# Optimization experiments

Hardware: AMD Instinct MI355X
Metric: run time of the kernel (lower is better)

Reference implementation:

```python
import jax, jax.numpy as jnp
import numpy as np

DIM = 1024
CTX_DIM = 768
H = 16


def setup_inputs() -> dict:
    key = jax.random.key(0)
    k1, k2, k3, k4, k5 = jax.random.split(key, 5)
    x = jax.random.normal(k1, (2, 2048, DIM), dtype=jnp.float32)
    context = jax.random.normal(k2, (2, 2048, CTX_DIM), dtype=jnp.float32)
    # Linear weights stored as [in, out] (y = x @ W); no biases per module.
    s = 0.02
    Wq = jax.random.normal(k3, (DIM, DIM), dtype=jnp.float32) * s
    Wkv = jax.random.normal(k4, (CTX_DIM, 2 * DIM), dtype=jnp.float32) * s
    Wo = jax.random.normal(k5, (DIM, DIM), dtype=jnp.float32) * s
    return {"x": x, "context": context, "Wq": Wq, "Wkv": Wkv, "Wo": Wo}


def reference(x, context, Wq, Wkv, Wo):
    B, N, C = x.shape
    Dh = C // H  # head dim
    scale = Dh ** -0.5
    M = context.shape[1]
    q = (x @ Wq).reshape(B, N, H, Dh).transpose(0, 2, 1, 3)      # [B,H,N,Dh]
    kv = context @ Wkv                                            # [B,M,2C]
    k, v = jnp.split(kv, 2, axis=-1)
    k = k.reshape(B, M, H, Dh).transpose(0, 2, 1, 3)              # [B,H,M,Dh]
    v = v.reshape(B, M, H, Dh).transpose(0, 2, 1, 3)              # [B,H,M,Dh]
    attn = jax.nn.softmax(jnp.einsum('bhnd,bhmd->bhnm', q, k) * scale, axis=-1)
    out = jnp.einsum('bhnm,bhmd->bhnd', attn, v)                  # [B,H,N,Dh]
    out = out.transpose(0, 2, 1, 3).reshape(B, N, C)
    return out @ Wo  # dropout is identity in eval / p=0
```

## Files before the change

### kernel.cpp

```cpp
#include <hip/hip_runtime.h>

typedef __attribute__((ext_vector_type(4))) float f32x4;
typedef __attribute__((ext_vector_type(8))) short short8;
typedef __attribute__((ext_vector_type(4))) unsigned int u32x4;
typedef unsigned short u16;
typedef unsigned int u32;
typedef unsigned long long u64;

__device__ __forceinline__ u16 f2bf(float f) {
  u32 u = __builtin_bit_cast(u32, f);
  u += 0x7fffu + ((u >> 16) & 1u);
  return (u16)(u >> 16);
}
__device__ __forceinline__ u16 f2bf_t(float f) {
  return (u16)(__builtin_bit_cast(u32, f) >> 16);
}

__device__ __forceinline__ void gl2lds16(const u16* g, const u16* l) {
  __builtin_amdgcn_global_load_lds(
      (const __attribute__((address_space(1))) u32*)g,
      (__attribute__((address_space(3))) u32*)(u32)(u64)l,
      16, 0, 0);
}

__device__ __forceinline__ void cast_body(const float* __restrict__ s,
                                          u16* __restrict__ d, int blk,
                                          int tid) {
  long i = (long)blk * 256 + tid;
  const f32x4* sp = (const f32x4*)(s + i * 8);
  f32x4 a = sp[0], b = sp[1];
  u16 t[8];
#pragma unroll
  for (int j = 0; j < 4; j++) {
    t[j] = f2bf(a[j]);
    t[4 + j] = f2bf(b[j]);
  }
  *(u32x4*)(d + i * 8) = *(u32x4*)t;
}

__device__ __forceinline__ void transpose_body(const float* __restrict__ W,
                                               u16* __restrict__ WT, int K,
                                               int N, int k0, int n0, int tid,
                                               u16* T) {
#pragma unroll
  for (int i = 0; i < 4; i++) {
    int c = tid + 256 * i;
    int row = c >> 4;
    int ch = c & 15;
    f32x4 f = *(const f32x4*)(W + (long)(k0 + row) * N + n0 + ch * 4);
#pragma unroll
    for (int j = 0; j < 4; j++) T[(ch * 4 + j) * 72 + row] = f2bf(f[j]);
  }
  __syncthreads();
#pragma unroll
  for (int i = 0; i < 2; i++) {
    int c = tid + 256 * i;
    int row = c >> 3;
    int ch = c & 7;
    u32x4 v = *(u32x4*)&T[row * 72 + ch * 8];
    *(u32x4*)(WT + (long)(n0 + row) * K + k0 + ch * 8) = v;
  }
}

__global__ __launch_bounds__(256) void prep(
    const float* __restrict__ x, const float* __restrict__ ctx,
    const float* __restrict__ Wq, const float* __restrict__ Wkv,
    const float* __restrict__ Wo, u16* __restrict__ xb,
    u16* __restrict__ ctxb, u16* __restrict__ wqT, u16* __restrict__ wkvT,
    u16* __restrict__ woT) {
  __shared__ __align__(16) u16 T[64 * 72];
  const int b = blockIdx.x, tid = threadIdx.x;
  if (b < 2048) {
    cast_body(x, xb, b, tid);
  } else if (b < 3584) {
    cast_body(ctx, ctxb, b - 2048, tid);
  } else if (b < 3840) {
    int idx = b - 3584;
    transpose_body(Wq, wqT, 1024, 1024, (idx >> 4) * 64, (idx & 15) * 64, tid, T);
  } else if (b < 4224) {
    int idx = b - 3840;
    transpose_body(Wkv, wkvT, 768, 2048, (idx >> 5) * 64, (idx & 31) * 64, tid, T);
  } else {
    int idx = b - 4224;
    transpose_body(Wo, woT, 1024, 1024, (idx >> 4) * 64, (idx & 15) * 64, tid, T);
  }
}

__device__ __forceinline__ void gemm128_core(
    const u16* __restrict__ A, const u16* __restrict__ Bt, int Kstride,
    int Klen, long brow, long bcol, int tid, u16* As, u16* Bs,
    f32x4 (&acc)[4][4]) {
  const int lane = tid & 63, wv = tid >> 6;
  const int l15 = lane & 15, quad = lane >> 4;
  const int wr = (wv >> 1) * 64, wc = (wv & 1) * 64;
  const int sr = lane >> 3, sc = lane & 7;
  const int csw = ((sc ^ sr) & 7) * 8;

  const u16* ag[4];
  const u16* bg[4];
  const u16* al[4];
  const u16* bl[4];
#pragma unroll
  for (int n = 0; n < 4; n++) {
    int row = wv * 32 + n * 8;
    ag[n] = A + (brow + row + sr) * (long)Kstride + csw;
    al[n] = &As[row * 64];
    bg[n] = Bt + (bcol + row + sr) * (long)Kstride + csw;
    bl[n] = &Bs[row * 64];
  }

  for (int kt = 0; kt < Klen; kt += 64) {
    __syncthreads();
#pragma unroll
    for (int n = 0; n < 4; n++) gl2lds16(ag[n] + kt, al[n]);
#pragma unroll
    for (int n = 0; n < 4; n++) gl2lds16(bg[n] + kt, bl[n]);
    __syncthreads();
#pragma unroll
    for (int kk = 0; kk < 2; kk++) {
      short8 af[4], bf[4];
#pragma unroll
      for (int i = 0; i < 4; i++) {
        int row = wr + i * 16 + l15;
        af[i] = *(short8*)&As[row * 64 + (((kk * 4 + quad) ^ (row & 7)) << 3)];
      }
#pragma unroll
      for (int j = 0; j < 4; j++) {
        int row = wc + j * 16 + l15;
        bf[j] = *(short8*)&Bs[row * 64 + (((kk * 4 + quad) ^ (row & 7)) << 3)];
      }
#pragma unroll
      for (int i = 0; i < 4; i++)
#pragma unroll
        for (int j = 0; j < 4; j++)
          acc[i][j] = __builtin_amdgcn_mfma_f32_16x16x32_bf16(
              af[i], bf[j], acc[i][j], 0, 0, 0);
    }
  }
}

__global__ __launch_bounds__(256, 3) void fused_qkv(
    const u16* __restrict__ xb, const u16* __restrict__ ctxb,
    const u16* __restrict__ wqT, const u16* __restrict__ wkvT,
    u16* __restrict__ Qb, u16* __restrict__ Kfrag, u16* __restrict__ Vfrag,
    float qscale) {
  __shared__ __align__(16) u16 As[128 * 64];
  __shared__ __align__(16) u16 Bs[128 * 64];
  const int tid = threadIdx.x;
  const int lane = tid & 63, wv = tid >> 6;
  const int l15 = lane & 15, quad = lane >> 4;
  const int wr = (wv >> 1) * 64, wc = (wv & 1) * 64;

  f32x4 acc[4][4];
#pragma unroll
  for (int i = 0; i < 4; i++)
#pragma unroll
    for (int j = 0; j < 4; j++) acc[i][j] = (f32x4){0.f, 0.f, 0.f, 0.f};

  int bid = blockIdx.x;
  if (bid < 256) {
    long brow = (long)(bid >> 3) * 128, bcol = (long)(bid & 7) * 128;
    gemm128_core(xb, wqT, 1024, 1024, brow, bcol, tid, As, Bs, acc);
#pragma unroll
    for (int i = 0; i < 4; i++)
#pragma unroll
      for (int j = 0; j < 4; j++)
#pragma unroll
        for (int r = 0; r < 4; r++) {
          long row = brow + wr + i * 16 + quad * 4 + r;
          long col = bcol + wc + j * 16 + l15;
          Qb[row * 1024 + col] = f2bf(acc[i][j][r] * qscale);
        }
    return;
  }

  bid -= 256;
  long brow = (long)(bid >> 4) * 128, bcol = (long)(bid & 15) * 128;
  gemm128_core(ctxb, wkvT, 768, 768, brow, bcol, tid, As, Bs, acc);

  const bool is_k = (bcol < 1024);
  __syncthreads();
#pragma unroll
  for (int round = 0; round < 2; round++) {
    if ((wv >> 1) == round) {
      if (is_k) {
#pragma unroll
        for (int i = 0; i < 4; i++)
#pragma unroll
          for (int j = 0; j < 4; j++) {
            int d = j * 16 + l15;
            int off = (wv & 1) * 4096 + ((d >> 5) * 4 + i) * 512 +
                      (((d >> 3) & 3) * 16 + quad * 4) * 8 + (d & 7);
#pragma unroll
            for (int r = 0; r < 4; r++) As[off + r * 8] = f2bf(acc[i][j][r]);
          }
      } else {
#pragma unroll
        for (int i = 0; i < 4; i++)
#pragma unroll
          for (int j = 0; j < 4; j++) {
            int off = (wv & 1) * 4096 + ((i >> 1) * 4 + j) * 512 +
                      (quad * 16 + l15) * 8 + (i & 1) * 4;
            u16 t4[4];
#pragma unroll
            for (int r = 0; r < 4; r++) t4[r] = f2bf(acc[i][j][r]);
            *(u64*)&As[off] = *(const u64*)t4;
          }
      }
    }
    __syncthreads();
    long mg = brow + round * 64;
    int b_ = (int)(mg >> 11), mt = (int)((mg >> 6) & 31);
#pragma unroll
    for (int h2 = 0; h2 < 2; h2++) {
      int h = (int)((is_k ? bcol : bcol - 1024) >> 6) + h2;
      u16* dst = (is_k ? Kfrag : Vfrag) + ((long)(b_ * 16 + h) * 32 + mt) * 4096;
#pragma unroll
      for (int p = 0; p < 2; p++) {
        int c = p * 256 + tid;
        *(u32x4*)(dst + c * 8) = *(u32x4*)&As[h2 * 4096 + c * 8];
      }
    }
    __syncthreads();
  }
}

__global__ __launch_bounds__(256, 3) void gemm_o(
    const u16* __restrict__ A, const u16* __restrict__ Bt,
    float* __restrict__ C) {
  __shared__ __align__(16) u16 As[128 * 64];
  __shared__ __align__(16) u16 Bs[128 * 64];
  const int tid = threadIdx.x;
  const int lane = tid & 63, wv = tid >> 6;
  const int l15 = lane & 15, quad = lane >> 4;
  const int wr = (wv >> 1) * 64, wc = (wv & 1) * 64;
  long brow = (long)blockIdx.y * 128, bcol = (long)blockIdx.x * 128;

  f32x4 acc[4][4];
#pragma unroll
  for (int i = 0; i < 4; i++)
#pragma unroll
    for (int j = 0; j < 4; j++) acc[i][j] = (f32x4){0.f, 0.f, 0.f, 0.f};

  gemm128_core(A, Bt, 1024, 1024, brow, bcol, tid, As, Bs, acc);

#pragma unroll
  for (int i = 0; i < 4; i++)
#pragma unroll
    for (int j = 0; j < 4; j++)
#pragma unroll
      for (int r = 0; r < 4; r++) {
        long row = brow + wr + i * 16 + quad * 4 + r;
        long col = bcol + wc + j * 16 + l15;
        C[row * 1024 + col] = acc[i][j][r];
      }
}

__global__ __launch_bounds__(512, 4) void attn_kernel(
    const u16* __restrict__ Q, const u16* __restrict__ Kfrag,
    const u16* __restrict__ Vfrag, u16* __restrict__ AO) {
  __shared__ __align__(16) u16 smem[2][4][4096];
  const int tid = threadIdx.x;
  const int lane = tid & 63, wv = tid >> 6;
  const int qc = wv & 3, half = wv >> 2;
  const int l15 = lane & 15, quad = lane >> 4;
  const int bh = blockIdx.y;
  const int b = bh >> 4, h = bh & 15;
  const long qrow0 = (long)b * 2048 + blockIdx.x * 128 + qc * 32;

  short8 qf[2][2];
#pragma unroll
  for (int qt = 0; qt < 2; qt++)
#pragma unroll
    for (int kk = 0; kk < 2; kk++)
      qf[qt][kk] = *(const short8*)&Q[(qrow0 + qt * 16 + l15) * 1024 +
                                      h * 64 + kk * 32 + quad * 8];

  f32x4 O[2][5];
#pragma unroll
  for (int qt = 0; qt < 2; qt++)
#pragma unroll
    for (int dt = 0; dt < 5; dt++) O[qt][dt] = (f32x4){0.f, 0.f, 0.f, 0.f};

  u32x4 ones_u = {0x3F803F80u, 0x3F803F80u, 0x3F803F80u, 0x3F803F80u};
  short8 ones = __builtin_bit_cast(short8, ones_u);

  const u16* kg0 = Kfrag + (long)bh * 32 * 4096;
  const u16* vg0 = Vfrag + (long)bh * 32 * 4096;
  const int so = wv * 512 + lane * 8;

  auto stage = [&](int nb, int i) {
    const u16* k0 = kg0 + (long)i * 4096 + so;
    const u16* v0 = vg0 + (long)i * 4096 + so;
    gl2lds16(k0, &smem[nb][0][wv * 512]);
    gl2lds16(v0, &smem[nb][1][wv * 512]);
    gl2lds16(k0 + 16 * 4096, &smem[nb][2][wv * 512]);
    gl2lds16(v0 + 16 * 4096, &smem[nb][3][wv * 512]);
  };

  stage(0, 0);
  __syncthreads();

  for (int i = 0; i < 16; i++) {
    const int cur = i & 1;
    if (i < 15) stage(cur ^ 1, i + 1);

    const u16* Ks = &smem[cur][half * 2][0] + lane * 8;
    const u16* Vs = &smem[cur][half * 2 + 1][0] + lane * 8;

    f32x4 s[4][2];
#pragma unroll
    for (int m4 = 0; m4 < 4; m4++)
#pragma unroll
      for (int qt = 0; qt < 2; qt++) s[m4][qt] = (f32x4){0.f, 0.f, 0.f, 0.f};
#pragma unroll
    for (int kk = 0; kk < 2; kk++) {
      short8 kf[4];
#pragma unroll
      for (int t = 0; t < 4; t++)
        kf[t] = *(const short8*)(Ks + (kk * 4 + t) * 512);
#pragma unroll
      for (int m4 = 0; m4 < 4; m4++)
#pragma unroll
        for (int qt = 0; qt < 2; qt++)
          s[m4][qt] = __builtin_amdgcn_mfma_f32_16x16x32_bf16(
              kf[m4], qf[qt][kk], s[m4][qt], 0, 0, 0);
    }

#pragma unroll
    for (int kk = 0; kk < 2; kk++) {
      short8 vf[4];
#pragma unroll
      for (int dt = 0; dt < 4; dt++)
        vf[dt] = *(const short8*)(Vs + (kk * 4 + dt) * 512);
#pragma unroll
      for (int qt = 0; qt < 2; qt++) {
        u32 w[4];
#pragma unroll
        for (int hw = 0; hw < 2; hw++) {
          f32x4 sv = s[2 * kk + hw][qt];
          u32 lo = (u32)f2bf_t(__builtin_amdgcn_exp2f(sv[0] - 24.f)) |
                   ((u32)f2bf_t(__builtin_amdgcn_exp2f(sv[1] - 24.f)) << 16);
          u32 hi = (u32)f2bf_t(__builtin_amdgcn_exp2f(sv[2] - 24.f)) |
                   ((u32)f2bf_t(__builtin_amdgcn_exp2f(sv[3] - 24.f)) << 16);
          w[hw * 2] = lo;
          w[hw * 2 + 1] = hi;
        }
        short8 pa = __builtin_bit_cast(short8, *(u32x4*)w);
#pragma unroll
        for (int dt = 0; dt < 4; dt++)
          O[qt][dt] = __builtin_amdgcn_mfma_f32_16x16x32_bf16(
              pa, vf[dt], O[qt][dt], 0, 0, 0);
        O[qt][4] = __builtin_amdgcn_mfma_f32_16x16x32_bf16(
            pa, ones, O[qt][4], 0, 0, 0);
      }
    }
    __syncthreads();
  }

  f32x4* cb = (f32x4*)&smem[0][0][0];
  if (half) {
#pragma unroll
    for (int qt = 0; qt < 2; qt++)
#pragma unroll
      for (int dt = 0; dt < 5; dt++)
        cb[(qc * 64 + lane) * 10 + qt * 5 + dt] = O[qt][dt];
  }
  __syncthreads();
  if (!half) {
#pragma unroll
    for (int qt = 0; qt < 2; qt++)
#pragma unroll
      for (int dt = 0; dt < 5; dt++)
        O[qt][dt] += cb[(qc * 64 + lane) * 10 + qt * 5 + dt];

#pragma unroll
    for (int qt = 0; qt < 2; qt++) {
      float inv[4];
#pragma unroll
      for (int r = 0; r < 4; r++) inv[r] = 1.f / O[qt][4][r];
#pragma unroll
      for (int dt = 0; dt < 4; dt++)
#pragma unroll
        for (int r = 0; r < 4; r++) {
          long row = qrow0 + qt * 16 + quad * 4 + r;
          int col = h * 64 + dt * 16 + l15;
          AO[row * 1024 + col] = f2bf(O[qt][dt][r] * inv[r]);
        }
    }
  }
}

extern "C" void kernel_launch(void* const* d_in, const int* in_sizes, int n_in,
                              void* d_out, int out_size, void* d_ws,
                              size_t ws_size, hipStream_t stream) {
  const float* x = (const float*)d_in[0];
  const float* ctx = (const float*)d_in[1];
  const float* Wq = (const float*)d_in[2];
  const float* Wkv = (const float*)d_in[3];
  const float* Wo = (const float*)d_in[4];
  float* out = (float*)d_out;

  u16* ws = (u16*)d_ws;
  u16* wqT = ws;
  u16* wkvT = wqT + 1048576;
  u16* woT = wkvT + 1572864;
  u16* Qb = woT + 1048576;
  u16* Kfrag = Qb + 4194304;
  u16* Vfrag = Kfrag + 4194304;
  u16* xb = Vfrag + 4194304;
  u16* ctxb = xb + 4194304;
  u16* AOb = xb;

  const float qscale = 0.125f * 1.4426950408889634f;

  prep<<<dim3(4480), 256, 0, stream>>>(x, ctx, Wq, Wkv, Wo, xb, ctxb, wqT,
                                       wkvT, woT);

  fused_qkv<<<dim3(768), 256, 0, stream>>>(xb, ctxb, wqT, wkvT, Qb, Kfrag,
                                           Vfrag, qscale);

  attn_kernel<<<dim3(16, 32), 512, 0, stream>>>(Qb, Kfrag, Vfrag, AOb);

  gemm_o<<<dim3(8, 32), 256, 0, stream>>>(AOb, woT, out);
}
```

Measured before the change: 178.1 us.

## Deepen attention K/V staging to four-buffer ring with finer steps

Restructures the attention loop from 16 double-buffered iterations into 32 half-sized steps over a 4-slot LDS ring, with three stages kept in flight. Each step waits on a manual vmcnt counter and a raw barrier instead of a full __syncthreads. It also wraps the MFMA bursts in s_setprio and packs the bf16 truncation with v_perm. The aim is to hide global-to-LDS load latency and lower synchronization stalls, at the cost of fragile manual waitcnt bookkeeping. LDS usage stays the same.

```diff
diff --git a/kernel.cpp b/kernel.cpp
--- a/kernel.cpp
+++ b/kernel.cpp
@@ -259,7 +259,7 @@
 __global__ __launch_bounds__(512, 4) void attn_kernel(
     const u16* __restrict__ Q, const u16* __restrict__ Kfrag,
     const u16* __restrict__ Vfrag, u16* __restrict__ AO) {
-  __shared__ __align__(16) u16 smem[2][4][4096];
+  __shared__ __align__(16) u16 smem[4][8192];
   const int tid = threadIdx.x;
   const int lane = tid & 63, wv = tid >> 6;
   const int qc = wv & 3, half = wv >> 2;
@@ -287,78 +287,102 @@
 
   const u16* kg0 = Kfrag + (long)bh * 32 * 4096;
   const u16* vg0 = Vfrag + (long)bh * 32 * 4096;
-  const int so = wv * 512 + lane * 8;
-
-  auto stage = [&](int nb, int i) {
-    const u16* k0 = kg0 + (long)i * 4096 + so;
-    const u16* v0 = vg0 + (long)i * 4096 + so;
-    gl2lds16(k0, &smem[nb][0][wv * 512]);
-    gl2lds16(v0, &smem[nb][1][wv * 512]);
-    gl2lds16(k0 + 16 * 4096, &smem[nb][2][wv * 512]);
-    gl2lds16(v0 + 16 * 4096, &smem[nb][3][wv * 512]);
+
+  auto stage = [&](int s) {
+#pragma unroll
+    for (int u = 0; u < 2; u++) {
+      int c = wv * 2 + u;
+      int g3 = c >> 2, idx = c & 3;
+      int hh = g3 >> 1;
+      const u16* src;
+      if ((g3 & 1) == 0) {
+        int kk = idx >> 1, tt = idx & 1;
+        src = kg0 + (long)(hh * 16 + (s >> 1)) * 4096 +
+              (kk * 4 + (s & 1) * 2 + tt) * 512 + lane * 8;
+      } else {
+        src = vg0 + (long)(hh * 16 + (s >> 1)) * 4096 +
+              ((s & 1) * 4 + idx) * 512 + lane * 8;
+      }
+      gl2lds16(src, &smem[s & 3][c * 512]);
+    }
   };
 
-  stage(0, 0);
-  __syncthreads();
-
-  for (int i = 0; i < 16; i++) {
-    const int cur = i & 1;
-    if (i < 15) stage(cur ^ 1, i + 1);
-
-    const u16* Ks = &smem[cur][half * 2][0] + lane * 8;
-    const u16* Vs = &smem[cur][half * 2 + 1][0] + lane * 8;
-
-    f32x4 s[4][2];
-#pragma unroll
-    for (int m4 = 0; m4 < 4; m4++)
-#pragma unroll
-      for (int qt = 0; qt < 2; qt++) s[m4][qt] = (f32x4){0.f, 0.f, 0.f, 0.f};
-#pragma unroll
-    for (int kk = 0; kk < 2; kk++) {
-      short8 kf[4];
-#pragma unroll
-      for (int t = 0; t < 4; t++)
-        kf[t] = *(const short8*)(Ks + (kk * 4 + t) * 512);
-#pragma unroll
-      for (int m4 = 0; m4 < 4; m4++)
+  stage(0);
+  stage(1);
+  stage(2);
+
+  for (int s = 0; s < 32; s++) {
+    if (s < 30)
+      asm volatile("s_waitcnt vmcnt(4)" ::: "memory");
+    else if (s == 30)
+      asm volatile("s_waitcnt vmcnt(2)" ::: "memory");
+    else
+      asm volatile("s_waitcnt vmcnt(0)" ::: "memory");
+    __builtin_amdgcn_s_barrier();
+    asm volatile("" ::: "memory");
+    if (s + 3 < 32) stage(s + 3);
+
+    const u16* rb = &smem[s & 3][0];
+    const u16* Ks = rb + half * 4096 + lane * 8;
+    const u16* Vs = rb + half * 4096 + 2048 + lane * 8;
+
+    short8 kf[2][2];
+#pragma unroll
+    for (int kk = 0; kk < 2; kk++)
+#pragma unroll
+      for (int tt = 0; tt < 2; tt++)
+        kf[kk][tt] = *(const short8*)(Ks + (kk * 2 + tt) * 512);
+    f32x4 sacc[2][2];
+#pragma unroll
+    for (int tt = 0; tt < 2; tt++)
+#pragma unroll
+      for (int qt = 0; qt < 2; qt++) sacc[tt][qt] = (f32x4){0.f, 0.f, 0.f, 0.f};
+    __builtin_amdgcn_s_setprio(1);
+#pragma unroll
+    for (int kk = 0; kk < 2; kk++)
+#pragma unroll
+      for (int tt = 0; tt < 2; tt++)
 #pragma unroll
         for (int qt = 0; qt < 2; qt++)
-          s[m4][qt] = __builtin_amdgcn_mfma_f32_16x16x32_bf16(
-              kf[m4], qf[qt][kk], s[m4][qt], 0, 0, 0);
-    }
-
-#pragma unroll
-    for (int kk = 0; kk < 2; kk++) {
-      short8 vf[4];
+          sacc[tt][qt] = __builtin_amdgcn_mfma_f32_16x16x32_bf16(
+              kf[kk][tt], qf[qt][kk], sacc[tt][qt], 0, 0, 0);
+    __builtin_amdgcn_s_setprio(0);
+
+    short8 pa[2];
+#pragma unroll
+    for (int qt = 0; qt < 2; qt++) {
+      u32 w[4];
+#pragma unroll
+      for (int tt = 0; tt < 2; tt++) {
+        f32x4 sv = sacc[tt][qt];
+        u32 e0 = __builtin_bit_cast(u32, __builtin_amdgcn_exp2f(sv[0] - 24.f));
+        u32 e1 = __builtin_bit_cast(u32, __builtin_amdgcn_exp2f(sv[1] - 24.f));
+        u32 e2 = __builtin_bit_cast(u32, __builtin_amdgcn_exp2f(sv[2] - 24.f));
+        u32 e3 = __builtin_bit_cast(u32, __builtin_amdgcn_exp2f(sv[3] - 24.f));
+        w[tt * 2] = __builtin_amdgcn_perm(e1, e0, 0x07060302u);
+        w[tt * 2 + 1] = __builtin_amdgcn_perm(e3, e2, 0x07060302u);
+      }
+      pa[qt] = __builtin_bit_cast(short8, *(u32x4*)w);
+    }
+
+    short8 vf[4];
+#pragma unroll
+    for (int dt = 0; dt < 4; dt++)
+      vf[dt] = *(const short8*)(Vs + dt * 512);
+    __builtin_amdgcn_s_setprio(1);
+#pragma unroll
+    for (int qt = 0; qt < 2; qt++) {
 #pragma unroll
       for (int dt = 0; dt < 4; dt++)
-        vf[dt] = *(const short8*)(Vs + (kk * 4 + dt) * 512);
-#pragma unroll
-      for (int qt = 0; qt < 2; qt++) {
-        u32 w[4];
-#pragma unroll
-        for (int hw = 0; hw < 2; hw++) {
-          f32x4 sv = s[2 * kk + hw][qt];
-          u32 lo = (u32)f2bf_t(__builtin_amdgcn_exp2f(sv[0] - 24.f)) |
-                   ((u32)f2bf_t(__builtin_amdgcn_exp2f(sv[1] - 24.f)) << 16);
-          u32 hi = (u32)f2bf_t(__builtin_amdgcn_exp2f(sv[2] - 24.f)) |
-                   ((u32)f2bf_t(__builtin_amdgcn_exp2f(sv[3] - 24.f)) << 16);
-          w[hw * 2] = lo;
-          w[hw * 2 + 1] = hi;
-        }
-        short8 pa = __builtin_bit_cast(short8, *(u32x4*)w);
-#pragma unroll
-        for (int dt = 0; dt < 4; dt++)
-          O[qt][dt] = __builtin_amdgcn_mfma_f32_16x16x32_bf16(
-              pa, vf[dt], O[qt][dt], 0, 0, 0);
-        O[qt][4] = __builtin_amdgcn_mfma_f32_16x16x32_bf16(
-            pa, ones, O[qt][4], 0, 0, 0);
-      }
-    }
-    __syncthreads();
-  }
-
-  f32x4* cb = (f32x4*)&smem[0][0][0];
+        O[qt][dt] = __builtin_amdgcn_mfma_f32_16x16x32_bf16(
+            pa[qt], vf[dt], O[qt][dt], 0, 0, 0);
+      O[qt][4] = __builtin_amdgcn_mfma_f32_16x16x32_bf16(
+          pa[qt], ones, O[qt][4], 0, 0, 0);
+    }
+    __builtin_amdgcn_s_setprio(0);
+  }
+
+  f32x4* cb = (f32x4*)&smem[0][0];
   if (half) {
 #pragma unroll
     for (int qt = 0; qt < 2; qt++)
```

Measured after the change: 181.6 us. Within noise of the previous version (+1.9%).
